# Performance work log

Measured on AMD Instinct MI355X. Metric: run time of the kernel, lower is better.

## Reference

```python
import jax, jax.numpy as jnp
import numpy as np

TAU = 2.0
THETA_BASE = 0.5
SURROGATE_ALPHA = 4.0


def setup_inputs() -> dict:
    key = jax.random.key(0)
    x = jax.random.normal(key, (1024, 32, 1024), dtype=jnp.float32)  # (T, B, F)
    return {"x": x}


def reference(x):
    # Linear recurrence I[t] = decay * I[t-1] + x[t], I[-1] = 0,
    # solved with a log-depth associative scan (matches forward_parallel /
    # matmul_recursive in the torch module, and forward(use_deer=True)).
    decay = jnp.exp(jnp.asarray(-1.0 / TAU, dtype=x.dtype))
    a = jnp.full_like(x, decay)  # per-step decay coefficient

    def combine(c1, c2):
        a1, b1 = c1
        a2, b2 = c2
        return (a1 * a2, a2 * b1 + b2)

    _, I = jax.lax.associative_scan(combine, (a, x), axis=0)  # (T, B, F)
    # Surrogate sigmoid spike (used in both train and eval per _compute_spikes_adaptive)
    spike = jax.nn.sigmoid(SURROGATE_ALPHA * (I - THETA_BASE))
    return spike
```

## Files before the change

kernel.cpp:

```cpp
#include <hip/hip_runtime.h>


#define T_DIM   1024
#define B_DIM   32
#define F_DIM   1024
#define LCHUNK  16
#define KHALO   24
#define F4_DIM  (F_DIM / 4)
#define SEQ4    (B_DIM * F4_DIM)
#define NCHUNK  (T_DIM / LCHUNK)
#define GDEPTH  8

typedef float f32x4 __attribute__((ext_vector_type(4)));

__device__ __forceinline__ float spike1(float I) {
    float z = fmaf(-4.0f, I, 2.0f);
    float e = __expf(z);
    return __builtin_amdgcn_rcpf(1.0f + e);
}

__device__ __forceinline__ f32x4 spike4(f32x4 I) {
    f32x4 r;
    r.x = spike1(I.x); r.y = spike1(I.y); r.z = spike1(I.z); r.w = spike1(I.w);
    return r;
}

__global__ __launch_bounds__(256, 8) void lif_scan_kernel(
        const f32x4* __restrict__ x, f32x4* __restrict__ out) {
    const float d = 0.60653065971263342f;

    int tid   = blockIdx.x * 256 + threadIdx.x;
    int s     = tid & (SEQ4 - 1);
    int chunk = tid >> 13;

    int t0    = chunk * LCHUNK;
    int nwarm = (t0 < KHALO) ? t0 : KHALO;
    int idx   = (t0 - nwarm) * SEQ4 + s;

    f32x4 I = (f32x4)(0.0f);

    #pragma unroll 1
    for (int g = 0; g < nwarm / GDEPTH; ++g) {
        f32x4 a[GDEPTH];
        #pragma unroll
        for (int j = 0; j < GDEPTH; ++j) a[j] = x[idx + j * SEQ4];
        #pragma unroll
        for (int j = 0; j < GDEPTH; ++j) I = d * I + a[j];
        idx += GDEPTH * SEQ4;
    }

    #pragma unroll 1
    for (int g = 0; g < LCHUNK / GDEPTH; ++g) {
        f32x4 a[GDEPTH];
        #pragma unroll
        for (int j = 0; j < GDEPTH; ++j) a[j] = x[idx + j * SEQ4];
        #pragma unroll
        for (int j = 0; j < GDEPTH; ++j) {
            I = d * I + a[j];
            __builtin_nontemporal_store(spike4(I), &out[idx + j * SEQ4]);
        }
        idx += GDEPTH * SEQ4;
    }
}

extern "C" void kernel_launch(void* const* d_in, const int* in_sizes, int n_in,
                              void* d_out, int out_size, void* d_ws, size_t ws_size,
                              hipStream_t stream) {
    const f32x4* x   = (const f32x4*)d_in[0];
    f32x4*       out = (f32x4*)d_out;
    int total_threads = NCHUNK * SEQ4;
    dim3 grid(total_threads / 256), block(256);
    lif_scan_kernel<<<grid, block, 0, stream>>>(x, out);
}
```

Baseline: 238.4 us.

## Shrink warm-up halo to 16 and double-buffer fully unrolled loads

Cuts the warm-up halo for each 16-step chunk from 24 to 16 timesteps, which reduces redundant reads of x. It fully unrolls the warm-up and output phases with two register buffers so the next group's loads are issued while the current group is accumulated. It special-cases the first chunk and lowers the launch-bounds occupancy hint from 8 to 6 to leave room for the extra registers. The shorter halo truncates the recurrence earlier (decay^16 ≈ 3e-4 instead of decay^24 ≈ 6e-6), which raises numerical error slightly.

```diff
diff --git a/kernel.cpp b/kernel.cpp
--- a/kernel.cpp
+++ b/kernel.cpp
@@ -5,11 +5,11 @@
 #define B_DIM   32
 #define F_DIM   1024
 #define LCHUNK  16
-#define KHALO   24
+#define KHALO   16
 #define F4_DIM  (F_DIM / 4)
 #define SEQ4    (B_DIM * F4_DIM)
 #define NCHUNK  (T_DIM / LCHUNK)
-#define GDEPTH  8
+#define G       8
 
 typedef float f32x4 __attribute__((ext_vector_type(4)));
 
@@ -25,41 +25,60 @@
     return r;
 }
 
-__global__ __launch_bounds__(256, 8) void lif_scan_kernel(
+__global__ __launch_bounds__(256, 6) void lif_scan_kernel(
         const f32x4* __restrict__ x, f32x4* __restrict__ out) {
     const float d = 0.60653065971263342f;
 
     int tid   = blockIdx.x * 256 + threadIdx.x;
     int s     = tid & (SEQ4 - 1);
     int chunk = tid >> 13;
-
     int t0    = chunk * LCHUNK;
-    int nwarm = (t0 < KHALO) ? t0 : KHALO;
-    int idx   = (t0 - nwarm) * SEQ4 + s;
 
     f32x4 I = (f32x4)(0.0f);
+    f32x4 a[G], b[G];
 
-    #pragma unroll 1
-    for (int g = 0; g < nwarm / GDEPTH; ++g) {
-        f32x4 a[GDEPTH];
+    if (t0 == 0) {
         #pragma unroll
-        for (int j = 0; j < GDEPTH; ++j) a[j] = x[idx + j * SEQ4];
+        for (int j = 0; j < G; ++j) a[j] = x[s + j * SEQ4];
         #pragma unroll
-        for (int j = 0; j < GDEPTH; ++j) I = d * I + a[j];
-        idx += GDEPTH * SEQ4;
-    }
+        for (int j = 0; j < G; ++j) b[j] = x[s + (G + j) * SEQ4];
+        #pragma unroll
+        for (int j = 0; j < G; ++j) {
+            I = d * I + a[j];
+            __builtin_nontemporal_store(spike4(I), &out[s + j * SEQ4]);
+        }
+        #pragma unroll
+        for (int j = 0; j < G; ++j) {
+            I = d * I + b[j];
+            __builtin_nontemporal_store(spike4(I), &out[s + (G + j) * SEQ4]);
+        }
+    } else {
+        int li = (t0 - KHALO) * SEQ4 + s;
+        #pragma unroll
+        for (int j = 0; j < G; ++j) a[j] = x[li + j * SEQ4];
+        #pragma unroll
+        for (int j = 0; j < G; ++j) b[j] = x[li + (G + j) * SEQ4];
 
-    #pragma unroll 1
-    for (int g = 0; g < LCHUNK / GDEPTH; ++g) {
-        f32x4 a[GDEPTH];
         #pragma unroll
-        for (int j = 0; j < GDEPTH; ++j) a[j] = x[idx + j * SEQ4];
+        for (int j = 0; j < G; ++j) I = d * I + a[j];
         #pragma unroll
-        for (int j = 0; j < GDEPTH; ++j) {
+        for (int j = 0; j < G; ++j) a[j] = x[li + (2 * G + j) * SEQ4];
+        #pragma unroll
+        for (int j = 0; j < G; ++j) I = d * I + b[j];
+        #pragma unroll
+        for (int j = 0; j < G; ++j) b[j] = x[li + (3 * G + j) * SEQ4];
+
+        int si = t0 * SEQ4 + s;
+        #pragma unroll
+        for (int j = 0; j < G; ++j) {
             I = d * I + a[j];
-            __builtin_nontemporal_store(spike4(I), &out[idx + j * SEQ4]);
+            __builtin_nontemporal_store(spike4(I), &out[si + j * SEQ4]);
         }
-        idx += GDEPTH * SEQ4;
+        #pragma unroll
+        for (int j = 0; j < G; ++j) {
+            I = d * I + b[j];
+            __builtin_nontemporal_store(spike4(I), &out[si + (G + j) * SEQ4]);
+        }
     }
 }
 
```

Result: faster. 229.0 us (-4.0%).
